# Optimization experiments

Measured on AMD Instinct MI355X. Metric: run time of the kernel, lower is better.

## Reference

```python
import jax, jax.numpy as jnp
import numpy as np

B, T, D, H, O = 256, 512, 256, 1024, 128


def setup_inputs() -> dict:
    key = jax.random.key(0)
    ks = jax.random.split(key, 16)
    s_x = 1.0 / np.sqrt(D)
    s_h = 1.0 / np.sqrt(H)
    def lin(k, shape, s):
        return jax.random.uniform(k, shape, jnp.float32, -s, s)
    return {
        "x": jax.random.normal(ks[0], (B, T, D), jnp.float32),
        "Wgx": lin(ks[1], (H, D), s_x), "bgx": lin(ks[2], (H,), s_x),
        "Wgh": lin(ks[3], (H, H), s_h),
        "Wix": lin(ks[4], (H, D), s_x), "bix": lin(ks[5], (H,), s_x),
        "Wih": lin(ks[6], (H, H), s_h),
        "Wfx": lin(ks[7], (H, D), s_x), "bfx": lin(ks[8], (H,), s_x),
        "Wfh": lin(ks[9], (H, H), s_h),
        "Wox": lin(ks[10], (H, D), s_x), "box": lin(ks[11], (H,), s_x),
        "Woh": lin(ks[12], (H, H), s_h),
        "Why": lin(ks[13], (O, H), s_h), "bhy": lin(ks[14], (O,), s_h),
    }


def _lstm_forward(x, Wgx, bgx, Wgh, Wix, bix, Wih, Wfx, bfx, Wfh, Wox, box, Woh, Why, bhy):
    # Precompute all input-side projections in one big GEMM: [B,T,4H]
    Wx = jnp.concatenate([Wgx, Wix, Wfx, Wox], axis=0)          # [4H, D]
    bx = jnp.concatenate([bgx, bix, bfx, box], axis=0)          # [4H]
    Wh = jnp.concatenate([Wgh, Wih, Wfh, Woh], axis=0)          # [4H, H]
    xz = jnp.einsum('btd,kd->tbk', x, Wx) + bx                  # [T,B,4H]

    Hd = Wgh.shape[0]

    def step(carry, xz_t):
        h, c = carry
        z = xz_t + h @ Wh.T                                     # [B,4H]
        g = jnp.tanh(z[:, :Hd])
        i = jax.nn.sigmoid(z[:, Hd:2 * Hd])
        f = jax.nn.sigmoid(z[:, 2 * Hd:3 * Hd])
        o = jax.nn.sigmoid(z[:, 3 * Hd:])
        c = g * i + c * f
        h = jnp.tanh(c) * o
        return (h, c), None

    h0 = jnp.zeros((x.shape[0], Hd), x.dtype)
    c0 = jnp.zeros((x.shape[0], Hd), x.dtype)
    (h, _), _ = jax.lax.scan(step, (h0, c0), xz)
    p = h @ Why.T + bhy
    return jax.nn.softmax(p, axis=-1)


def reference(x, Wgx, bgx, Wgh, Wix, bix, Wih, Wfx, bfx, Wfh, Wox, box, Woh, Why, bhy):
    return _lstm_forward(x, Wgx, bgx, Wgh, Wix, bix, Wih, Wfx, bfx, Wfh, Wox, box, Woh, Why, bhy)
```

## Files before the change

kernel.cpp:

```cpp
#include <hip/hip_runtime.h>
#include <math.h>

#define B_  256
#define T_  512
#define D_  256
#define H_  1024
#define O_  128
#define N4H 4096

typedef __attribute__((ext_vector_type(8))) short bf16x8;
typedef __attribute__((ext_vector_type(4))) float f32x4;

__device__ __forceinline__ unsigned short f2bf(float x) {
    union { float f; unsigned u; } v; v.f = x;
    unsigned r = v.u + 0x7fffu + ((v.u >> 16) & 1u);
    return (unsigned short)(r >> 16);
}
__device__ __forceinline__ float bf2f(unsigned short b) {
    union { float f; unsigned u; } v; v.u = ((unsigned)b) << 16;
    return v.f;
}
__device__ __forceinline__ void splitf(float w, short& hi, short& lo) {
    union { float f; unsigned u; } v; v.f = w;
    union { float f; unsigned u; } hf; hf.u = v.u & 0xffff0000u;
    hi = (short)(unsigned short)(v.u >> 16);
    lo = (short)f2bf(w - hf.f);
}

__device__ __forceinline__ void load_h_batch(
    const unsigned short* a0, const unsigned short* a1,
    const unsigned short* a2, const unsigned short* a3,
    const unsigned short* b0, const unsigned short* b1,
    const unsigned short* b2, const unsigned short* b3,
    bf16x8& r0, bf16x8& r1, bf16x8& r2, bf16x8& r3,
    bf16x8& r4, bf16x8& r5, bf16x8& r6, bf16x8& r7)
{
    asm volatile(
        "global_load_dwordx4 %0, %8, off sc0 sc1\n\t"
        "global_load_dwordx4 %1, %9, off sc0 sc1\n\t"
        "global_load_dwordx4 %2, %10, off sc0 sc1\n\t"
        "global_load_dwordx4 %3, %11, off sc0 sc1\n\t"
        "global_load_dwordx4 %4, %12, off sc0 sc1\n\t"
        "global_load_dwordx4 %5, %13, off sc0 sc1\n\t"
        "global_load_dwordx4 %6, %14, off sc0 sc1\n\t"
        "global_load_dwordx4 %7, %15, off sc0 sc1\n\t"
        "s_waitcnt vmcnt(0)"
        : "=&v"(r0), "=&v"(r1), "=&v"(r2), "=&v"(r3),
          "=&v"(r4), "=&v"(r5), "=&v"(r6), "=&v"(r7)
        : "v"(a0), "v"(a1), "v"(a2), "v"(a3),
          "v"(b0), "v"(b1), "v"(b2), "v"(b3)
        : "memory");
}

__device__ __forceinline__ void store_h4(unsigned short* p, unsigned int d) {
    asm volatile("global_store_dword %0, %1, off sc0 sc1"
                 :: "v"(p), "v"(d) : "memory");
}

__global__ __launch_bounds__(256) void pack_weights(
    const float* __restrict__ Wgx, const float* __restrict__ bgx, const float* __restrict__ Wgh,
    const float* __restrict__ Wix, const float* __restrict__ bix, const float* __restrict__ Wih,
    const float* __restrict__ Wfx, const float* __restrict__ bfx, const float* __restrict__ Wfh,
    const float* __restrict__ Wox, const float* __restrict__ box, const float* __restrict__ Woh,
    unsigned short* __restrict__ Whhi, unsigned short* __restrict__ Whlo,
    unsigned short* __restrict__ WXhi, unsigned short* __restrict__ WXlo,
    float* __restrict__ biasP)
{
    int idx = blockIdx.x * 256 + threadIdx.x;
    const int K = H_ + D_;
    const int total = N4H * K;
    if (idx < total) {
        int np = idx / K;
        int k  = idx - np * K;
        int j = np >> 2, g = np & 3;
        const float* Wh = (g == 0) ? Wgh : (g == 1) ? Wih : (g == 2) ? Wfh : Woh;
        const float* Wx = (g == 0) ? Wgx : (g == 1) ? Wix : (g == 2) ? Wfx : Wox;
        float w = (k < H_) ? Wh[j * H_ + k] : Wx[j * D_ + (k - H_)];
        unsigned short hi = f2bf(w);
        unsigned short lo = f2bf(w - bf2f(hi));
        if (k < H_) { Whhi[np * H_ + k] = hi; Whlo[np * H_ + k] = lo; }
        else        { WXhi[np * D_ + (k - H_)] = hi; WXlo[np * D_ + (k - H_)] = lo; }
    }
    if (idx < N4H) {
        int j = idx >> 2, g = idx & 3;
        const float* bx = (g == 0) ? bgx : (g == 1) ? bix : (g == 2) ? bfx : box;
        biasP[idx] = bx[j];
    }
}

__global__ __launch_bounds__(512, 2) void lstm_persistent(
    const float* __restrict__ x,
    const unsigned short* __restrict__ Whhi, const unsigned short* __restrict__ Whlo,
    const unsigned short* __restrict__ WXhi, const unsigned short* __restrict__ WXlo,
    const float* __restrict__ biasP,
    unsigned short* __restrict__ h0hi, unsigned short* __restrict__ h0lo,
    unsigned short* __restrict__ h1hi, unsigned short* __restrict__ h1lo,
    float* __restrict__ xz,
    unsigned int* __restrict__ bar,
    int Tc)
{
    __shared__ __align__(16) float zbuf[8][64][68];

    const int tid  = threadIdx.x;
    const int wave = tid >> 6;
    const int lane = tid & 63;
    const int lrow = lane & 15;
    const int quad = lane >> 4;

    const int fid = blockIdx.x;
    const int xcd = fid & 7;
    const int s   = fid >> 3;
    const int cgi = xcd * 8 + (s & 7);
    const int rg  = s >> 3;
    const int rbase = rg * 64;
    const int cbase = cgi * 64;

    const int b_loc = tid >> 3;
    const int oc    = (tid & 7) * 8;
    const int bown  = rbase + b_loc;
    const int j0    = cgi * 16 + (tid & 7) * 2;
    float c0 = 0.f, c1 = 0.f;

    unsigned int* const mybar = bar + rg * 32;
    unsigned int barTarget = 0;

    for (int t0 = 0; t0 < T_; t0 += Tc) {
        const int tc = (T_ - t0 < Tc) ? (T_ - t0) : Tc;

        for (int t_rel = wave; t_rel < tc; t_rel += 8) {
            const int t = t0 + t_rel;
            f32x4 acc[4][4];
            #pragma unroll
            for (int rs = 0; rs < 4; ++rs)
                #pragma unroll
                for (int cs = 0; cs < 4; ++cs)
                    acc[rs][cs] = (f32x4){0.f, 0.f, 0.f, 0.f};

            #pragma unroll 1
            for (int kc = 0; kc < D_; kc += 32) {
                bf16x8 Ahi[4], Alo[4], Bh[4], Bl[4];
                #pragma unroll
                for (int rs = 0; rs < 4; ++rs) {
                    int b = rbase + rs * 16 + lrow;
                    const float* p = x + (size_t)b * (T_ * D_) + (size_t)t * D_ + kc + quad * 8;
                    float4 v0 = *(const float4*)p;
                    float4 v1 = *(const float4*)(p + 4);
                    float vv[8] = {v0.x, v0.y, v0.z, v0.w, v1.x, v1.y, v1.z, v1.w};
                    #pragma unroll
                    for (int j = 0; j < 8; ++j) {
                        short hi, lo; splitf(vv[j], hi, lo);
                        Ahi[rs][j] = hi; Alo[rs][j] = lo;
                    }
                }
                #pragma unroll
                for (int cs = 0; cs < 4; ++cs) {
                    int off = (cbase + cs * 16 + lrow) * D_ + kc + quad * 8;
                    Bh[cs] = *(const bf16x8*)(WXhi + off);
                    Bl[cs] = *(const bf16x8*)(WXlo + off);
                }
                #pragma unroll
                for (int rs = 0; rs < 4; ++rs)
                    #pragma unroll
                    for (int cs = 0; cs < 4; ++cs) {
                        acc[rs][cs] = __builtin_amdgcn_mfma_f32_16x16x32_bf16(Ahi[rs], Bh[cs], acc[rs][cs], 0, 0, 0);
                        acc[rs][cs] = __builtin_amdgcn_mfma_f32_16x16x32_bf16(Ahi[rs], Bl[cs], acc[rs][cs], 0, 0, 0);
                        acc[rs][cs] = __builtin_amdgcn_mfma_f32_16x16x32_bf16(Alo[rs], Bh[cs], acc[rs][cs], 0, 0, 0);
                    }
            }
            #pragma unroll
            for (int cs = 0; cs < 4; ++cs) {
                int col = cbase + cs * 16 + lrow;
                float bv = biasP[col];
                #pragma unroll
                for (int rs = 0; rs < 4; ++rs) {
                    int row0 = rbase + rs * 16 + quad * 4;
                    #pragma unroll
                    for (int r = 0; r < 4; ++r)
                        xz[(size_t)(t_rel * B_ + row0 + r) * N4H + col] = acc[rs][cs][r] + bv;
                }
            }
        }

        for (int t_rel = 0; t_rel < tc; ++t_rel) {
            const int t = t0 + t_rel;
            const unsigned short* ih = (t & 1) ? h1hi : h0hi;
            const unsigned short* il = (t & 1) ? h1lo : h0lo;
            unsigned short* oh = (t & 1) ? h0hi : h1hi;
            unsigned short* ol = (t & 1) ? h0lo : h1lo;

            f32x4 acc[4][4];
            #pragma unroll
            for (int rs = 0; rs < 4; ++rs)
                #pragma unroll
                for (int cs = 0; cs < 4; ++cs)
                    acc[rs][cs] = (f32x4){0.f, 0.f, 0.f, 0.f};

            const int kb = wave * 128;
            #pragma unroll 1
            for (int kc = 0; kc < 128; kc += 32) {
                const int k = kb + kc + quad * 8;
                bf16x8 Ahi[4], Alo[4], Bh[4], Bl[4];
                #pragma unroll
                for (int cs = 0; cs < 4; ++cs) {
                    int off = (cbase + cs * 16 + lrow) * H_ + k;
                    Bh[cs] = *(const bf16x8*)(Whhi + off);
                    Bl[cs] = *(const bf16x8*)(Whlo + off);
                }
                const int r0o = (rbase + 0 * 16 + lrow) * H_ + k;
                const int r1o = (rbase + 1 * 16 + lrow) * H_ + k;
                const int r2o = (rbase + 2 * 16 + lrow) * H_ + k;
                const int r3o = (rbase + 3 * 16 + lrow) * H_ + k;
                load_h_batch(ih + r0o, ih + r1o, ih + r2o, ih + r3o,
                             il + r0o, il + r1o, il + r2o, il + r3o,
                             Ahi[0], Ahi[1], Ahi[2], Ahi[3],
                             Alo[0], Alo[1], Alo[2], Alo[3]);
                #pragma unroll
                for (int rs = 0; rs < 4; ++rs)
                    #pragma unroll
                    for (int cs = 0; cs < 4; ++cs) {
                        acc[rs][cs] = __builtin_amdgcn_mfma_f32_16x16x32_bf16(Ahi[rs], Bh[cs], acc[rs][cs], 0, 0, 0);
                        acc[rs][cs] = __builtin_amdgcn_mfma_f32_16x16x32_bf16(Ahi[rs], Bl[cs], acc[rs][cs], 0, 0, 0);
                        acc[rs][cs] = __builtin_amdgcn_mfma_f32_16x16x32_bf16(Alo[rs], Bh[cs], acc[rs][cs], 0, 0, 0);
                    }
            }

            #pragma unroll
            for (int rs = 0; rs < 4; ++rs)
                #pragma unroll
                for (int cs = 0; cs < 4; ++cs)
                    #pragma unroll
                    for (int r = 0; r < 4; ++r)
                        zbuf[wave][rs * 16 + quad * 4 + r][cs * 16 + lrow] = acc[rs][cs][r];
            __syncthreads();

            float zz[8];
            #pragma unroll
            for (int i = 0; i < 8; i += 4) {
                float s0 = 0.f, s1 = 0.f, s2 = 0.f, s3 = 0.f;
                #pragma unroll
                for (int w = 0; w < 8; ++w) {
                    float4 v = *(const float4*)&zbuf[w][b_loc][oc + i];
                    s0 += v.x; s1 += v.y; s2 += v.z; s3 += v.w;
                }
                zz[i] = s0; zz[i + 1] = s1; zz[i + 2] = s2; zz[i + 3] = s3;
            }

            const size_t xzoff = ((size_t)t_rel * B_ + bown) * N4H + cbase + oc;
            float4 xa = *(const float4*)(xz + xzoff);
            float4 xb = *(const float4*)(xz + xzoff + 4);
            zz[0] += xa.x; zz[1] += xa.y; zz[2] += xa.z; zz[3] += xa.w;
            zz[4] += xb.x; zz[5] += xb.y; zz[6] += xb.z; zz[7] += xb.w;

            float cold[2] = {c0, c1};
            unsigned short hh[2], hl[2];
            float cnew[2];
            #pragma unroll
            for (int j = 0; j < 2; ++j) {
                float zg = zz[4 * j + 0];
                float zi = zz[4 * j + 1];
                float zf = zz[4 * j + 2];
                float zo = zz[4 * j + 3];
                float g  = tanhf(zg);
                float ig = 1.f / (1.f + expf(-zi));
                float fg = 1.f / (1.f + expf(-zf));
                float og = 1.f / (1.f + expf(-zo));
                float cn = g * ig + cold[j] * fg;
                float hn = tanhf(cn) * og;
                cnew[j] = cn;
                unsigned short h16 = f2bf(hn);
                hh[j] = h16;
                hl[j] = f2bf(hn - bf2f(h16));
            }
            c0 = cnew[0]; c1 = cnew[1];
            store_h4(&oh[bown * H_ + j0], (unsigned)hh[0] | ((unsigned)hh[1] << 16));
            store_h4(&ol[bown * H_ + j0], (unsigned)hl[0] | ((unsigned)hl[1] << 16));

            __syncthreads();
            if (t != T_ - 1) {
                barTarget += 64;
                if (tid == 0) {
                    __hip_atomic_fetch_add(mybar, 1u, __ATOMIC_RELAXED,
                                           __HIP_MEMORY_SCOPE_AGENT);
                    while (__hip_atomic_load(mybar, __ATOMIC_RELAXED,
                                             __HIP_MEMORY_SCOPE_AGENT) < barTarget)
                        __builtin_amdgcn_s_sleep(1);
                }
                __syncthreads();
            }
        }
    }
}

__global__ __launch_bounds__(128) void final_proj(
    const unsigned short* __restrict__ hhi, const unsigned short* __restrict__ hlo,
    const float* __restrict__ Why, const float* __restrict__ bhy,
    float* __restrict__ out)
{
    __shared__ float hsh[H_];
    __shared__ float red[O_];
    const int b = blockIdx.x, tid = threadIdx.x;

    for (int k = tid; k < H_; k += O_)
        hsh[k] = bf2f(hhi[(size_t)b * H_ + k]) + bf2f(hlo[(size_t)b * H_ + k]);
    __syncthreads();

    float s = bhy[tid];
    const float* w = Why + (size_t)tid * H_;
    #pragma unroll 4
    for (int k = 0; k < H_; k += 4) {
        float4 wv = *(const float4*)(w + k);
        s += hsh[k] * wv.x + hsh[k + 1] * wv.y + hsh[k + 2] * wv.z + hsh[k + 3] * wv.w;
    }

    red[tid] = s; __syncthreads();
    for (int off = 64; off > 0; off >>= 1) {
        if (tid < off) red[tid] = fmaxf(red[tid], red[tid + off]);
        __syncthreads();
    }
    float mx = red[0]; __syncthreads();
    float e = expf(s - mx);
    red[tid] = e; __syncthreads();
    for (int off = 64; off > 0; off >>= 1) {
        if (tid < off) red[tid] += red[tid + off];
        __syncthreads();
    }
    out[(size_t)b * O_ + tid] = e / red[0];
}

extern "C" void kernel_launch(void* const* d_in, const int* in_sizes, int n_in,
                              void* d_out, int out_size, void* d_ws, size_t ws_size,
                              hipStream_t stream)
{
    const float* x   = (const float*)d_in[0];
    const float* Wgx = (const float*)d_in[1];
    const float* bgx = (const float*)d_in[2];
    const float* Wgh = (const float*)d_in[3];
    const float* Wix = (const float*)d_in[4];
    const float* bix = (const float*)d_in[5];
    const float* Wih = (const float*)d_in[6];
    const float* Wfx = (const float*)d_in[7];
    const float* bfx = (const float*)d_in[8];
    const float* Wfh = (const float*)d_in[9];
    const float* Wox = (const float*)d_in[10];
    const float* box = (const float*)d_in[11];
    const float* Woh = (const float*)d_in[12];
    const float* Why = (const float*)d_in[13];
    const float* bhy = (const float*)d_in[14];

    unsigned short* Whhi = (unsigned short*)d_ws;
    unsigned short* Whlo = Whhi + (size_t)N4H * H_;
    unsigned short* WXhi = Whlo + (size_t)N4H * H_;
    unsigned short* WXlo = WXhi + (size_t)N4H * D_;
    float*          bP   = (float*)(WXlo + (size_t)N4H * D_);
    unsigned int*   bars = (unsigned int*)(bP + N4H);
    unsigned short* hA_hi = (unsigned short*)(bars + 128);
    unsigned short* hA_lo = hA_hi + (size_t)B_ * H_;
    unsigned short* hB_hi = hA_lo + (size_t)B_ * H_;
    unsigned short* hB_lo = hB_hi + (size_t)B_ * H_;
    float*          xz    = (float*)(hB_lo + (size_t)B_ * H_);

    const size_t fixed_bytes = (size_t)((char*)xz - (char*)d_ws);
    const size_t per_t = (size_t)B_ * N4H * sizeof(float);
    int Tc = 1;
    if (ws_size > fixed_bytes) {
        size_t fit = (ws_size - fixed_bytes) / per_t;
        Tc = (fit > 32) ? 32 : (fit < 1 ? 1 : (int)fit);
    }

    hipMemsetAsync(bars, 0, 512 + (size_t)B_ * H_ * 4, stream);

    const int totalW = N4H * (H_ + D_);
    pack_weights<<<(totalW + 255) / 256, 256, 0, stream>>>(
        Wgx, bgx, Wgh, Wix, bix, Wih, Wfx, bfx, Wfh, Wox, box, Woh,
        Whhi, Whlo, WXhi, WXlo, bP);

    void* kargs[] = {
        (void*)&x, (void*)&Whhi, (void*)&Whlo, (void*)&WXhi, (void*)&WXlo,
        (void*)&bP, (void*)&hA_hi, (void*)&hA_lo, (void*)&hB_hi, (void*)&hB_lo,
        (void*)&xz, (void*)&bars, (void*)&Tc
    };
    hipLaunchCooperativeKernel((const void*)lstm_persistent,
                               dim3(256), dim3(512), kargs, 0, stream);

    final_proj<<<B_, 128, 0, stream>>>(hA_hi, hA_lo, Why, bhy, (float*)d_out);
}
```

Measured before the change: 11.67 ms.

## Overlap input projection with recurrent barrier wait and retile blocks to 32x128

The input-side projection for the next time chunk now runs in small units inside the per-step barrier wait, instead of as a separate phase before each chunk. The xz buffer is double-buffered to make this possible. Tiles change from 64 rows x 64 cols to 32 rows x 128 cols, so each barrier group has 32 blocks instead of 64. The aim is to hide projection work behind the grid-sync latency and shrink barrier fan-in, at the cost of twice the xz workspace, possibly a smaller Tc, and more register pressure.

```diff
diff --git a/kernel.cpp b/kernel.cpp
--- a/kernel.cpp
+++ b/kernel.cpp
@@ -27,34 +27,29 @@
     lo = (short)f2bf(w - hf.f);
 }
 
-__device__ __forceinline__ void load_h_batch(
+__device__ __forceinline__ void load_h4(
     const unsigned short* a0, const unsigned short* a1,
-    const unsigned short* a2, const unsigned short* a3,
     const unsigned short* b0, const unsigned short* b1,
-    const unsigned short* b2, const unsigned short* b3,
-    bf16x8& r0, bf16x8& r1, bf16x8& r2, bf16x8& r3,
-    bf16x8& r4, bf16x8& r5, bf16x8& r6, bf16x8& r7)
+    bf16x8& r0, bf16x8& r1, bf16x8& r2, bf16x8& r3)
 {
     asm volatile(
-        "global_load_dwordx4 %0, %8, off sc0 sc1\n\t"
-        "global_load_dwordx4 %1, %9, off sc0 sc1\n\t"
-        "global_load_dwordx4 %2, %10, off sc0 sc1\n\t"
-        "global_load_dwordx4 %3, %11, off sc0 sc1\n\t"
-        "global_load_dwordx4 %4, %12, off sc0 sc1\n\t"
-        "global_load_dwordx4 %5, %13, off sc0 sc1\n\t"
-        "global_load_dwordx4 %6, %14, off sc0 sc1\n\t"
-        "global_load_dwordx4 %7, %15, off sc0 sc1\n\t"
+        "global_load_dwordx4 %0, %4, off sc0 sc1\n\t"
+        "global_load_dwordx4 %1, %5, off sc0 sc1\n\t"
+        "global_load_dwordx4 %2, %6, off sc0 sc1\n\t"
+        "global_load_dwordx4 %3, %7, off sc0 sc1\n\t"
         "s_waitcnt vmcnt(0)"
-        : "=&v"(r0), "=&v"(r1), "=&v"(r2), "=&v"(r3),
-          "=&v"(r4), "=&v"(r5), "=&v"(r6), "=&v"(r7)
-        : "v"(a0), "v"(a1), "v"(a2), "v"(a3),
-          "v"(b0), "v"(b1), "v"(b2), "v"(b3)
+        : "=&v"(r0), "=&v"(r1), "=&v"(r2), "=&v"(r3)
+        : "v"(a0), "v"(a1), "v"(b0), "v"(b1)
         : "memory");
 }
 
 __device__ __forceinline__ void store_h4(unsigned short* p, unsigned int d) {
     asm volatile("global_store_dword %0, %1, off sc0 sc1"
                  :: "v"(p), "v"(d) : "memory");
+}
+
+__device__ __forceinline__ void drain_vmem() {
+    asm volatile("s_waitcnt vmcnt(0)" ::: "memory");
 }
 
 __global__ __launch_bounds__(256) void pack_weights(
@@ -88,6 +83,83 @@
     }
 }
 
+struct Prod {
+    int t;
+    int u;
+    f32x4 xa[2][4];
+};
+
+__device__ __forceinline__ void prod_zero(Prod& P) {
+    #pragma unroll
+    for (int rs = 0; rs < 2; ++rs)
+        #pragma unroll
+        for (int cs = 0; cs < 4; ++cs)
+            P.xa[rs][cs] = (f32x4){0.f, 0.f, 0.f, 0.f};
+}
+
+__device__ __forceinline__ void prod_unit(
+    Prod& P, int tcn, int nt0,
+    const float* __restrict__ x,
+    const unsigned short* __restrict__ WXhi,
+    const unsigned short* __restrict__ WXlo,
+    const float* __restrict__ biasP,
+    float* __restrict__ xzn,
+    int rbase, int cbase, int lrow, int quad)
+{
+    if (P.t >= tcn) return;
+    const int kc   = (P.u & 7) * 32;
+    const int half = P.u >> 3;
+    const int t    = nt0 + P.t;
+
+    bf16x8 Ahi[2], Alo[2];
+    #pragma unroll
+    for (int rs = 0; rs < 2; ++rs) {
+        int b = rbase + rs * 16 + lrow;
+        const float* p = x + (size_t)b * (T_ * D_) + (size_t)t * D_ + kc + quad * 8;
+        float4 v0 = *(const float4*)p;
+        float4 v1 = *(const float4*)(p + 4);
+        float vv[8] = {v0.x, v0.y, v0.z, v0.w, v1.x, v1.y, v1.z, v1.w};
+        #pragma unroll
+        for (int j = 0; j < 8; ++j) {
+            short hi, lo; splitf(vv[j], hi, lo);
+            Ahi[rs][j] = hi; Alo[rs][j] = lo;
+        }
+    }
+    bf16x8 Bh[4], Bl[4];
+    #pragma unroll
+    for (int cs = 0; cs < 4; ++cs) {
+        int off = (cbase + half * 64 + cs * 16 + lrow) * D_ + kc + quad * 8;
+        Bh[cs] = *(const bf16x8*)(WXhi + off);
+        Bl[cs] = *(const bf16x8*)(WXlo + off);
+    }
+    #pragma unroll
+    for (int rs = 0; rs < 2; ++rs)
+        #pragma unroll
+        for (int cs = 0; cs < 4; ++cs) {
+            P.xa[rs][cs] = __builtin_amdgcn_mfma_f32_16x16x32_bf16(Ahi[rs], Bh[cs], P.xa[rs][cs], 0, 0, 0);
+            P.xa[rs][cs] = __builtin_amdgcn_mfma_f32_16x16x32_bf16(Ahi[rs], Bl[cs], P.xa[rs][cs], 0, 0, 0);
+            P.xa[rs][cs] = __builtin_amdgcn_mfma_f32_16x16x32_bf16(Alo[rs], Bh[cs], P.xa[rs][cs], 0, 0, 0);
+        }
+
+    P.u += 1;
+    if ((P.u & 7) == 0) {
+        #pragma unroll
+        for (int cs = 0; cs < 4; ++cs) {
+            int col = cbase + half * 64 + cs * 16 + lrow;
+            float bv = biasP[col];
+            #pragma unroll
+            for (int rs = 0; rs < 2; ++rs) {
+                int row0 = rbase + rs * 16 + quad * 4;
+                #pragma unroll
+                for (int r = 0; r < 4; ++r)
+                    xzn[(size_t)(P.t * B_ + row0 + r) * N4H + col] = P.xa[rs][cs][r] + bv;
+            }
+        }
+        prod_zero(P);
+        if (P.u == 16) { P.u = 0; P.t += 8; }
+    }
+}
+
 __global__ __launch_bounds__(512, 2) void lstm_persistent(
     const float* __restrict__ x,
     const unsigned short* __restrict__ Whhi, const unsigned short* __restrict__ Whlo,
@@ -95,11 +167,11 @@
     const float* __restrict__ biasP,
     unsigned short* __restrict__ h0hi, unsigned short* __restrict__ h0lo,
     unsigned short* __restrict__ h1hi, unsigned short* __restrict__ h1lo,
-    float* __restrict__ xz,
+    float* xzA, float* xzB,
     unsigned int* __restrict__ bar,
     int Tc)
 {
-    __shared__ __align__(16) float zbuf[8][64][68];
+    __shared__ __align__(16) float zbuf[8][32][132];
 
     const int tid  = threadIdx.x;
     const int wave = tid >> 6;
@@ -110,124 +182,94 @@
     const int fid = blockIdx.x;
     const int xcd = fid & 7;
     const int s   = fid >> 3;
-    const int cgi = xcd * 8 + (s & 7);
-    const int rg  = s >> 3;
-    const int rbase = rg * 64;
-    const int cbase = cgi * 64;
-
-    const int b_loc = tid >> 3;
-    const int oc    = (tid & 7) * 8;
+    const int cgi = xcd * 4 + (s & 3);
+    const int rg  = s >> 2;
+    const int rbase = rg * 32;
+    const int cbase = cgi * 128;
+
+    const int b_loc = tid >> 4;
+    const int cq    = tid & 15;
+    const int oc    = cq * 8;
     const int bown  = rbase + b_loc;
-    const int j0    = cgi * 16 + (tid & 7) * 2;
+    const int j0    = cgi * 32 + cq * 2;
     float c0 = 0.f, c1 = 0.f;
 
     unsigned int* const mybar = bar + rg * 32;
     unsigned int barTarget = 0;
 
-    for (int t0 = 0; t0 < T_; t0 += Tc) {
-        const int tc = (T_ - t0 < Tc) ? (T_ - t0) : Tc;
-
-        for (int t_rel = wave; t_rel < tc; t_rel += 8) {
-            const int t = t0 + t_rel;
-            f32x4 acc[4][4];
+    int t0 = 0, cur = 0;
+    int tcc = (Tc < T_) ? Tc : T_;
+
+    {
+        Prod P; P.t = wave; P.u = 0; prod_zero(P);
+        while (P.t < tcc)
+            prod_unit(P, tcc, 0, x, WXhi, WXlo, biasP, xzA,
+                      rbase, cbase, lrow, quad);
+    }
+    __syncthreads();
+
+    while (true) {
+        const int nt0 = t0 + tcc;
+        const int tcn = (nt0 < T_) ? ((T_ - nt0 < Tc) ? T_ - nt0 : Tc) : 0;
+        float* const xzc = cur ? xzB : xzA;
+        float* const xzn = cur ? xzA : xzB;
+
+        Prod P; P.t = wave; P.u = 0; prod_zero(P);
+        const int ntiles = (tcn > wave) ? ((tcn - wave + 7) >> 3) : 0;
+        const int units  = ntiles * 16;
+        const int Q      = (units + tcc - 1) / tcc;
+
+        for (int tr = 0; tr < tcc; ++tr) {
+            const int t = t0 + tr;
+            const unsigned short* ih = (t & 1) ? h1hi : h0hi;
+            const unsigned short* il = (t & 1) ? h1lo : h0lo;
+            unsigned short* oh = (t & 1) ? h0hi : h1hi;
+            unsigned short* ol = (t & 1) ? h0lo : h1lo;
+
+            f32x4 acc[2][8];
             #pragma unroll
-            for (int rs = 0; rs < 4; ++rs)
-                #pragma unroll
-                for (int cs = 0; cs < 4; ++cs)
+            for (int rs = 0; rs < 2; ++rs)
+                #pragma unroll
+                for (int cs = 0; cs < 8; ++cs)
                     acc[rs][cs] = (f32x4){0.f, 0.f, 0.f, 0.f};
 
+            const int kb = wave * 128;
             #pragma unroll 1
-            for (int kc = 0; kc < D_; kc += 32) {
-                bf16x8 Ahi[4], Alo[4], Bh[4], Bl[4];
-                #pragma unroll
-                for (int rs = 0; rs < 4; ++rs) {
-                    int b = rbase + rs * 16 + lrow;
-                    const float* p = x + (size_t)b * (T_ * D_) + (size_t)t * D_ + kc + quad * 8;
-                    float4 v0 = *(const float4*)p;
-                    float4 v1 = *(const float4*)(p + 4);
-                    float vv[8] = {v0.x, v0.y, v0.z, v0.w, v1.x, v1.y, v1.z, v1.w};
+            for (int kc4 = 0; kc4 < 4; ++kc4) {
+                const int k = kb + kc4 * 32 + quad * 8;
+                bf16x8 Ahi[2], Alo[2], Bh[8], Bl[8];
+                #pragma unroll
+                for (int cs = 0; cs < 4; ++cs) {
+                    int off = (cbase + cs * 16 + lrow) * H_ + k;
+                    Bh[cs] = *(const bf16x8*)(Whhi + off);
+                    Bl[cs] = *(const bf16x8*)(Whlo + off);
+                }
+                {
+                    int o0 = (rbase + 0 * 16 + lrow) * H_ + k;
+                    int o1 = (rbase + 1 * 16 + lrow) * H_ + k;
+                    load_h4(ih + o0, ih + o1, il + o0, il + o1,
+                            Ahi[0], Ahi[1], Alo[0], Alo[1]);
+                }
+                #pragma unroll
+                for (int cs = 4; cs < 8; ++cs) {
+                    int off = (cbase + cs * 16 + lrow) * H_ + k;
+                    Bh[cs] = *(const bf16x8*)(Whhi + off);
+                    Bl[cs] = *(const bf16x8*)(Whlo + off);
+                }
+                #pragma unroll
+                for (int rs = 0; rs < 2; ++rs)
                     #pragma unroll
-                    for (int j = 0; j < 8; ++j) {
-                        short hi, lo; splitf(vv[j], hi, lo);
-                        Ahi[rs][j] = hi; Alo[rs][j] = lo;
-                    }
-                }
-                #pragma unroll
-                for (int cs = 0; cs < 4; ++cs) {
-                    int off = (cbase + cs * 16 + lrow) * D_ + kc + quad * 8;
-                    Bh[cs] = *(const bf16x8*)(WXhi + off);
-                    Bl[cs] = *(const bf16x8*)(WXlo + off);
-                }
-                #pragma unroll
-                for (int rs = 0; rs < 4; ++rs)
-                    #pragma unroll
-                    for (int cs = 0; cs < 4; ++cs) {
+                    for (int cs = 0; cs < 8; ++cs) {
                         acc[rs][cs] = __builtin_amdgcn_mfma_f32_16x16x32_bf16(Ahi[rs], Bh[cs], acc[rs][cs], 0, 0, 0);
                         acc[rs][cs] = __builtin_amdgcn_mfma_f32_16x16x32_bf16(Ahi[rs], Bl[cs], acc[rs][cs], 0, 0, 0);
                         acc[rs][cs] = __builtin_amdgcn_mfma_f32_16x16x32_bf16(Alo[rs], Bh[cs], acc[rs][cs], 0, 0, 0);
                     }
             }
+
             #pragma unroll
-            for (int cs = 0; cs < 4; ++cs) {
-                int col = cbase + cs * 16 + lrow;
-                float bv = biasP[col];
-                #pragma unroll
-                for (int rs = 0; rs < 4; ++rs) {
-                    int row0 = rbase + rs * 16 + quad * 4;
-                    #pragma unroll
-                    for (int r = 0; r < 4; ++r)
-                        xz[(size_t)(t_rel * B_ + row0 + r) * N4H + col] = acc[rs][cs][r] + bv;
-                }
-            }
-        }
-
-        for (int t_rel = 0; t_rel < tc; ++t_rel) {
-            const int t = t0 + t_rel;
-            const unsigned short* ih = (t & 1) ? h1hi : h0hi;
-            const unsigned short* il = (t & 1) ? h1lo : h0lo;
-            unsigned short* oh = (t & 1) ? h0hi : h1hi;
-            unsigned short* ol = (t & 1) ? h0lo : h1lo;
-
-            f32x4 acc[4][4];
-            #pragma unroll
-            for (int rs = 0; rs < 4; ++rs)
-                #pragma unroll
-                for (int cs = 0; cs < 4; ++cs)
-                    acc[rs][cs] = (f32x4){0.f, 0.f, 0.f, 0.f};
-
-            const int kb = wave * 128;
-            #pragma unroll 1
-            for (int kc = 0; kc < 128; kc += 32) {
-                const int k = kb + kc + quad * 8;
-                bf16x8 Ahi[4], Alo[4], Bh[4], Bl[4];
-                #pragma unroll
-                for (int cs = 0; cs < 4; ++cs) {
-                    int off = (cbase + cs * 16 + lrow) * H_ + k;
-                    Bh[cs] = *(const bf16x8*)(Whhi + off);
-                    Bl[cs] = *(const bf16x8*)(Whlo + off);
-                }
-                const int r0o = (rbase + 0 * 16 + lrow) * H_ + k;
-                const int r1o = (rbase + 1 * 16 + lrow) * H_ + k;
-                const int r2o = (rbase + 2 * 16 + lrow) * H_ + k;
-                const int r3o = (rbase + 3 * 16 + lrow) * H_ + k;
-                load_h_batch(ih + r0o, ih + r1o, ih + r2o, ih + r3o,
-                             il + r0o, il + r1o, il + r2o, il + r3o,
-                             Ahi[0], Ahi[1], Ahi[2], Ahi[3],
-                             Alo[0], Alo[1], Alo[2], Alo[3]);
-                #pragma unroll
-                for (int rs = 0; rs < 4; ++rs)
-                    #pragma unroll
-                    for (int cs = 0; cs < 4; ++cs) {
-                        acc[rs][cs] = __builtin_amdgcn_mfma_f32_16x16x32_bf16(Ahi[rs], Bh[cs], acc[rs][cs], 0, 0, 0);
-                        acc[rs][cs] = __builtin_amdgcn_mfma_f32_16x16x32_bf16(Ahi[rs], Bl[cs], acc[rs][cs], 0, 0, 0);
-                        acc[rs][cs] = __builtin_amdgcn_mfma_f32_16x16x32_bf16(Alo[rs], Bh[cs], acc[rs][cs], 0, 0, 0);
-                    }
-            }
-
-            #pragma unroll
-            for (int rs = 0; rs < 4; ++rs)
-                #pragma unroll
-                for (int cs = 0; cs < 4; ++cs)
+            for (int rs = 0; rs < 2; ++rs)
+                #pragma unroll
+                for (int cs = 0; cs < 8; ++cs)
                     #pragma unroll
                     for (int r = 0; r < 4; ++r)
                         zbuf[wave][rs * 16 + quad * 4 + r][cs * 16 + lrow] = acc[rs][cs][r];
@@ -245,9 +287,9 @@
                 zz[i] = s0; zz[i + 1] = s1; zz[i + 2] = s2; zz[i + 3] = s3;
             }
 
-            const size_t xzoff = ((size_t)t_rel * B_ + bown) * N4H + cbase + oc;
-            float4 xa = *(const float4*)(xz + xzoff);
-            float4 xb = *(const float4*)(xz + xzoff + 4);
+            const size_t xzoff = ((size_t)tr * B_ + bown) * N4H + cbase + oc;
+            float4 xa = *(const float4*)(xzc + xzoff);
+            float4 xb = *(const float4*)(xzc + xzoff + 4);
             zz[0] += xa.x; zz[1] += xa.y; zz[2] += xa.z; zz[3] += xa.w;
             zz[4] += xb.x; zz[5] += xb.y; zz[6] += xb.z; zz[7] += xb.w;
 
@@ -275,12 +317,18 @@
             store_h4(&oh[bown * H_ + j0], (unsigned)hh[0] | ((unsigned)hh[1] << 16));
             store_h4(&ol[bown * H_ + j0], (unsigned)hl[0] | ((unsigned)hl[1] << 16));
 
+            drain_vmem();
             __syncthreads();
+
             if (t != T_ - 1) {
-                barTarget += 64;
-                if (tid == 0) {
+                barTarget += 32;
+                if (tid == 0)
                     __hip_atomic_fetch_add(mybar, 1u, __ATOMIC_RELAXED,
                                            __HIP_MEMORY_SCOPE_AGENT);
+                for (int q = 0; q < Q; ++q)
+                    prod_unit(P, tcn, nt0, x, WXhi, WXlo, biasP, xzn,
+                              rbase, cbase, lrow, quad);
+                if (tid == 0) {
                     while (__hip_atomic_load(mybar, __ATOMIC_RELAXED,
                                              __HIP_MEMORY_SCOPE_AGENT) < barTarget)
                         __builtin_amdgcn_s_sleep(1);
@@ -288,6 +336,9 @@
                 __syncthreads();
             }
         }
+
+        if (tcn == 0) break;
+        t0 = nt0; tcc = tcn; cur ^= 1;
     }
 }
 
@@ -353,21 +404,23 @@
     unsigned short* WXlo = WXhi + (size_t)N4H * D_;
     float*          bP   = (float*)(WXlo + (size_t)N4H * D_);
     unsigned int*   bars = (unsigned int*)(bP + N4H);
-    unsigned short* hA_hi = (unsigned short*)(bars + 128);
+    unsigned short* hA_hi = (unsigned short*)(bars + 1024);
     unsigned short* hA_lo = hA_hi + (size_t)B_ * H_;
     unsigned short* hB_hi = hA_lo + (size_t)B_ * H_;
     unsigned short* hB_lo = hB_hi + (size_t)B_ * H_;
-    float*          xz    = (float*)(hB_lo + (size_t)B_ * H_);
-
-    const size_t fixed_bytes = (size_t)((char*)xz - (char*)d_ws);
+    float*          xzBase = (float*)(hB_lo + (size_t)B_ * H_);
+
+    const size_t fixed_bytes = (size_t)((char*)xzBase - (char*)d_ws);
     const size_t per_t = (size_t)B_ * N4H * sizeof(float);
     int Tc = 1;
     if (ws_size > fixed_bytes) {
-        size_t fit = (ws_size - fixed_bytes) / per_t;
+        size_t fit = (ws_size - fixed_bytes) / (2 * per_t);
         Tc = (fit > 32) ? 32 : (fit < 1 ? 1 : (int)fit);
     }
-
-    hipMemsetAsync(bars, 0, 512 + (size_t)B_ * H_ * 4, stream);
+    float* xzA = xzBase;
+    float* xzB = xzBase + (size_t)Tc * B_ * N4H;
+
+    hipMemsetAsync(bars, 0, 4096 + (size_t)B_ * H_ * 4, stream);
 
     const int totalW = N4H * (H_ + D_);
     pack_weights<<<(totalW + 255) / 256, 256, 0, stream>>>(
@@ -377,7 +430,7 @@
     void* kargs[] = {
         (void*)&x, (void*)&Whhi, (void*)&Whlo, (void*)&WXhi, (void*)&WXlo,
         (void*)&bP, (void*)&hA_hi, (void*)&hA_lo, (void*)&hB_hi, (void*)&hB_lo,
-        (void*)&xz, (void*)&bars, (void*)&Tc
+        (void*)&xzA, (void*)&xzB, (void*)&bars, (void*)&Tc
     };
     hipLaunchCooperativeKernel((const void*)lstm_persistent,
                                dim3(256), dim3(512), kargs, 0, stream);
```

Result: slower. 13.61 ms (+16.6%).

## Retile LSTM recurrence to 32x128 blocks with LDS-staged h and per-block flags

Applied to the files above, without the earlier changes.

Each workgroup now owns 32 batch rows by 128 gate columns instead of 64x64. Each wave computes the full K=1024 reduction for its own 16 columns, so the cross-wave LDS reduction is gone. The h tile is staged once into swizzled LDS per step, and the atomic-counter barrier becomes per-block flag stores that wave 0 polls in parallel. The aim is to cut h global reloads, cross-wave reduction traffic and atomic contention on the per-step critical path. The cost is a larger LDS footprint and a flag scheme that relies on store visibility ordering.

```diff
diff --git a/kernel.cpp b/kernel.cpp
--- a/kernel.cpp
+++ b/kernel.cpp
@@ -27,28 +27,43 @@
     lo = (short)f2bf(w - hf.f);
 }
 
-__device__ __forceinline__ void load_h_batch(
-    const unsigned short* a0, const unsigned short* a1,
-    const unsigned short* a2, const unsigned short* a3,
-    const unsigned short* b0, const unsigned short* b1,
-    const unsigned short* b2, const unsigned short* b3,
+__device__ __forceinline__ void ld8_nowait(
+    const unsigned short* p,
     bf16x8& r0, bf16x8& r1, bf16x8& r2, bf16x8& r3,
     bf16x8& r4, bf16x8& r5, bf16x8& r6, bf16x8& r7)
 {
     asm volatile(
         "global_load_dwordx4 %0, %8, off sc0 sc1\n\t"
-        "global_load_dwordx4 %1, %9, off sc0 sc1\n\t"
-        "global_load_dwordx4 %2, %10, off sc0 sc1\n\t"
-        "global_load_dwordx4 %3, %11, off sc0 sc1\n\t"
-        "global_load_dwordx4 %4, %12, off sc0 sc1\n\t"
-        "global_load_dwordx4 %5, %13, off sc0 sc1\n\t"
-        "global_load_dwordx4 %6, %14, off sc0 sc1\n\t"
-        "global_load_dwordx4 %7, %15, off sc0 sc1\n\t"
+        "global_load_dwordx4 %1, %8, off offset:256 sc0 sc1\n\t"
+        "global_load_dwordx4 %2, %8, off offset:512 sc0 sc1\n\t"
+        "global_load_dwordx4 %3, %8, off offset:768 sc0 sc1\n\t"
+        "global_load_dwordx4 %4, %8, off offset:1024 sc0 sc1\n\t"
+        "global_load_dwordx4 %5, %8, off offset:1280 sc0 sc1\n\t"
+        "global_load_dwordx4 %6, %8, off offset:1536 sc0 sc1\n\t"
+        "global_load_dwordx4 %7, %8, off offset:1792 sc0 sc1"
+        : "=&v"(r0), "=&v"(r1), "=&v"(r2), "=&v"(r3),
+          "=&v"(r4), "=&v"(r5), "=&v"(r6), "=&v"(r7)
+        : "v"(p)
+        : "memory");
+}
+__device__ __forceinline__ void ld8_wait(
+    const unsigned short* p,
+    bf16x8& r0, bf16x8& r1, bf16x8& r2, bf16x8& r3,
+    bf16x8& r4, bf16x8& r5, bf16x8& r6, bf16x8& r7)
+{
+    asm volatile(
+        "global_load_dwordx4 %0, %8, off sc0 sc1\n\t"
+        "global_load_dwordx4 %1, %8, off offset:256 sc0 sc1\n\t"
+        "global_load_dwordx4 %2, %8, off offset:512 sc0 sc1\n\t"
+        "global_load_dwordx4 %3, %8, off offset:768 sc0 sc1\n\t"
+        "global_load_dwordx4 %4, %8, off offset:1024 sc0 sc1\n\t"
+        "global_load_dwordx4 %5, %8, off offset:1280 sc0 sc1\n\t"
+        "global_load_dwordx4 %6, %8, off offset:1536 sc0 sc1\n\t"
+        "global_load_dwordx4 %7, %8, off offset:1792 sc0 sc1\n\t"
         "s_waitcnt vmcnt(0)"
         : "=&v"(r0), "=&v"(r1), "=&v"(r2), "=&v"(r3),
           "=&v"(r4), "=&v"(r5), "=&v"(r6), "=&v"(r7)
-        : "v"(a0), "v"(a1), "v"(a2), "v"(a3),
-          "v"(b0), "v"(b1), "v"(b2), "v"(b3)
+        : "v"(p)
         : "memory");
 }
 
@@ -56,6 +71,21 @@
     asm volatile("global_store_dword %0, %1, off sc0 sc1"
                  :: "v"(p), "v"(d) : "memory");
 }
+__device__ __forceinline__ unsigned ld_flag(const unsigned* p) {
+    unsigned v;
+    asm volatile("global_load_dword %0, %1, off sc0 sc1\n\ts_waitcnt vmcnt(0)"
+                 : "=v"(v) : "v"(p) : "memory");
+    return v;
+}
+__device__ __forceinline__ void st_flag(unsigned* p, unsigned v) {
+    asm volatile("global_store_dword %0, %1, off sc0 sc1"
+                 :: "v"(p), "v"(v) : "memory");
+}
+__device__ __forceinline__ void drain_vmem() {
+    asm volatile("s_waitcnt vmcnt(0)" ::: "memory");
+}
+
+#define HIDX(k8, row) (((((k8) * 32) + (row)) * 8) ^ (((k8) & 7) * 8))
 
 __global__ __launch_bounds__(256) void pack_weights(
     const float* __restrict__ Wgx, const float* __restrict__ bgx, const float* __restrict__ Wgh,
@@ -96,10 +126,12 @@
     unsigned short* __restrict__ h0hi, unsigned short* __restrict__ h0lo,
     unsigned short* __restrict__ h1hi, unsigned short* __restrict__ h1lo,
     float* __restrict__ xz,
-    unsigned int* __restrict__ bar,
+    unsigned int* __restrict__ flg,
     int Tc)
 {
-    __shared__ __align__(16) float zbuf[8][64][68];
+    __shared__ __align__(16) unsigned short hsHI[32768];
+    __shared__ __align__(16) unsigned short hsLO[32768];
+    __shared__ __align__(16) float zsc[8][32][20];
 
     const int tid  = threadIdx.x;
     const int wave = tid >> 6;
@@ -110,150 +142,164 @@
     const int fid = blockIdx.x;
     const int xcd = fid & 7;
     const int s   = fid >> 3;
-    const int cgi = xcd * 8 + (s & 7);
-    const int rg  = s >> 3;
-    const int rbase = rg * 64;
-    const int cbase = cgi * 64;
-
-    const int b_loc = tid >> 3;
-    const int oc    = (tid & 7) * 8;
-    const int bown  = rbase + b_loc;
-    const int j0    = cgi * 16 + (tid & 7) * 2;
+    const int cgi = xcd * 4 + (s & 3);
+    const int rg  = s >> 2;
+    const int rbase = rg * 32;
+    const int cbase = cgi * 128;
+
+    const int srow = (tid >> 2) & 31;
+    const int sks  = (tid & 3) | (((tid >> 7) & 3) << 2);
+
+    const int erow = lane >> 1;
+    const int eps  = lane & 1;
+    const int bown = rbase + erow;
+    const int j0   = cgi * 32 + wave * 4 + eps * 2;
     float c0 = 0.f, c1 = 0.f;
 
-    unsigned int* const mybar = bar + rg * 32;
-    unsigned int barTarget = 0;
+    unsigned int* const myflag = flg + rg * 32 + cgi;
+    const unsigned int* const pollbase = flg + rg * 32;
 
     for (int t0 = 0; t0 < T_; t0 += Tc) {
         const int tc = (T_ - t0 < Tc) ? (T_ - t0) : Tc;
 
-        for (int t_rel = wave; t_rel < tc; t_rel += 8) {
-            const int t = t0 + t_rel;
-            f32x4 acc[4][4];
-            #pragma unroll
-            for (int rs = 0; rs < 4; ++rs)
+        for (int tr = wave; tr < tc; tr += 8) {
+            const int t = t0 + tr;
+            #pragma unroll 1
+            for (int hf = 0; hf < 2; ++hf) {
+                f32x4 xacc[2][4];
                 #pragma unroll
-                for (int cs = 0; cs < 4; ++cs)
-                    acc[rs][cs] = (f32x4){0.f, 0.f, 0.f, 0.f};
-
-            #pragma unroll 1
-            for (int kc = 0; kc < D_; kc += 32) {
-                bf16x8 Ahi[4], Alo[4], Bh[4], Bl[4];
-                #pragma unroll
-                for (int rs = 0; rs < 4; ++rs) {
-                    int b = rbase + rs * 16 + lrow;
-                    const float* p = x + (size_t)b * (T_ * D_) + (size_t)t * D_ + kc + quad * 8;
-                    float4 v0 = *(const float4*)p;
-                    float4 v1 = *(const float4*)(p + 4);
-                    float vv[8] = {v0.x, v0.y, v0.z, v0.w, v1.x, v1.y, v1.z, v1.w};
+                for (int rs = 0; rs < 2; ++rs)
                     #pragma unroll
-                    for (int j = 0; j < 8; ++j) {
-                        short hi, lo; splitf(vv[j], hi, lo);
-                        Ahi[rs][j] = hi; Alo[rs][j] = lo;
+                    for (int cs = 0; cs < 4; ++cs)
+                        xacc[rs][cs] = (f32x4){0.f, 0.f, 0.f, 0.f};
+                #pragma unroll 1
+                for (int kc = 0; kc < 8; ++kc) {
+                    const int kx = kc * 32 + quad * 8;
+                    bf16x8 Ahi[2], Alo[2];
+                    #pragma unroll
+                    for (int rs = 0; rs < 2; ++rs) {
+                        const float* p = x + (size_t)(rbase + rs * 16 + lrow) * (T_ * D_)
+                                           + (size_t)t * D_ + kx;
+                        float4 v0 = *(const float4*)p;
+                        float4 v1 = *(const float4*)(p + 4);
+                        float vv[8] = {v0.x, v0.y, v0.z, v0.w, v1.x, v1.y, v1.z, v1.w};
+                        #pragma unroll
+                        for (int j = 0; j < 8; ++j) {
+                            short hi, lo; splitf(vv[j], hi, lo);
+                            Ahi[rs][j] = hi; Alo[rs][j] = lo;
+                        }
                     }
+                    bf16x8 Bh[4], Bl[4];
+                    #pragma unroll
+                    for (int cs = 0; cs < 4; ++cs) {
+                        size_t off = (size_t)(cbase + hf * 64 + cs * 16 + lrow) * D_ + kx;
+                        Bh[cs] = *(const bf16x8*)(WXhi + off);
+                        Bl[cs] = *(const bf16x8*)(WXlo + off);
+                    }
+                    #pragma unroll
+                    for (int rs = 0; rs < 2; ++rs)
+                        #pragma unroll
+                        for (int cs = 0; cs < 4; ++cs) {
+                            xacc[rs][cs] = __builtin_amdgcn_mfma_f32_16x16x32_bf16(Ahi[rs], Bh[cs], xacc[rs][cs], 0, 0, 0);
+                            xacc[rs][cs] = __builtin_amdgcn_mfma_f32_16x16x32_bf16(Ahi[rs], Bl[cs], xacc[rs][cs], 0, 0, 0);
+                            xacc[rs][cs] = __builtin_amdgcn_mfma_f32_16x16x32_bf16(Alo[rs], Bh[cs], xacc[rs][cs], 0, 0, 0);
+                        }
                 }
                 #pragma unroll
                 for (int cs = 0; cs < 4; ++cs) {
-                    int off = (cbase + cs * 16 + lrow) * D_ + kc + quad * 8;
-                    Bh[cs] = *(const bf16x8*)(WXhi + off);
-                    Bl[cs] = *(const bf16x8*)(WXlo + off);
+                    int col = cbase + hf * 64 + cs * 16 + lrow;
+                    float bv = biasP[col];
+                    #pragma unroll
+                    for (int rs = 0; rs < 2; ++rs) {
+                        int row0 = rbase + rs * 16 + quad * 4;
+                        #pragma unroll
+                        for (int r = 0; r < 4; ++r)
+                            xz[(size_t)(tr * B_ + row0 + r) * N4H + col] = xacc[rs][cs][r] + bv;
+                    }
                 }
-                #pragma unroll
-                for (int rs = 0; rs < 4; ++rs)
-                    #pragma unroll
-                    for (int cs = 0; cs < 4; ++cs) {
-                        acc[rs][cs] = __builtin_amdgcn_mfma_f32_16x16x32_bf16(Ahi[rs], Bh[cs], acc[rs][cs], 0, 0, 0);
-                        acc[rs][cs] = __builtin_amdgcn_mfma_f32_16x16x32_bf16(Ahi[rs], Bl[cs], acc[rs][cs], 0, 0, 0);
-                        acc[rs][cs] = __builtin_amdgcn_mfma_f32_16x16x32_bf16(Alo[rs], Bh[cs], acc[rs][cs], 0, 0, 0);
-                    }
-            }
-            #pragma unroll
-            for (int cs = 0; cs < 4; ++cs) {
-                int col = cbase + cs * 16 + lrow;
-                float bv = biasP[col];
-                #pragma unroll
-                for (int rs = 0; rs < 4; ++rs) {
-                    int row0 = rbase + rs * 16 + quad * 4;
-                    #pragma unroll
-                    for (int r = 0; r < 4; ++r)
-                        xz[(size_t)(t_rel * B_ + row0 + r) * N4H + col] = acc[rs][cs][r] + bv;
-                }
             }
         }
-
-        for (int t_rel = 0; t_rel < tc; ++t_rel) {
-            const int t = t0 + t_rel;
+        __syncthreads();
+
+        for (int tr = 0; tr < tc; ++tr) {
+            const int t = t0 + tr;
             const unsigned short* ih = (t & 1) ? h1hi : h0hi;
             const unsigned short* il = (t & 1) ? h1lo : h0lo;
             unsigned short* oh = (t & 1) ? h0hi : h1hi;
             unsigned short* ol = (t & 1) ? h0lo : h1lo;
 
-            f32x4 acc[4][4];
+            {
+                const unsigned short* phi = ih + (size_t)(rbase + srow) * H_ + sks * 8;
+                const unsigned short* plo = il + (size_t)(rbase + srow) * H_ + sks * 8;
+                bf16x8 H0, H1, H2, H3, H4, H5, H6, H7;
+                bf16x8 L0, L1, L2, L3, L4, L5, L6, L7;
+                ld8_nowait(phi, H0, H1, H2, H3, H4, H5, H6, H7);
+                ld8_wait  (plo, L0, L1, L2, L3, L4, L5, L6, L7);
+                *(bf16x8*)&hsHI[HIDX(sks +   0, srow)] = H0;
+                *(bf16x8*)&hsHI[HIDX(sks +  16, srow)] = H1;
+                *(bf16x8*)&hsHI[HIDX(sks +  32, srow)] = H2;
+                *(bf16x8*)&hsHI[HIDX(sks +  48, srow)] = H3;
+                *(bf16x8*)&hsHI[HIDX(sks +  64, srow)] = H4;
+                *(bf16x8*)&hsHI[HIDX(sks +  80, srow)] = H5;
+                *(bf16x8*)&hsHI[HIDX(sks +  96, srow)] = H6;
+                *(bf16x8*)&hsHI[HIDX(sks + 112, srow)] = H7;
+                *(bf16x8*)&hsLO[HIDX(sks +   0, srow)] = L0;
+                *(bf16x8*)&hsLO[HIDX(sks +  16, srow)] = L1;
+                *(bf16x8*)&hsLO[HIDX(sks +  32, srow)] = L2;
+                *(bf16x8*)&hsLO[HIDX(sks +  48, srow)] = L3;
+                *(bf16x8*)&hsLO[HIDX(sks +  64, srow)] = L4;
+                *(bf16x8*)&hsLO[HIDX(sks +  80, srow)] = L5;
+                *(bf16x8*)&hsLO[HIDX(sks +  96, srow)] = L6;
+                *(bf16x8*)&hsLO[HIDX(sks + 112, srow)] = L7;
+            }
+            __syncthreads();
+
+            f32x4 aH0 = (f32x4){0.f,0.f,0.f,0.f}, aL0 = aH0, aX0 = aH0;
+            f32x4 aH1 = aH0, aL1 = aH0, aX1 = aH0;
+            {
+                const unsigned short* wbh = Whhi + (size_t)(cbase + wave * 16 + lrow) * H_ + quad * 8;
+                const unsigned short* wbl = Whlo + (size_t)(cbase + wave * 16 + lrow) * H_ + quad * 8;
+                #pragma unroll 4
+                for (int kc = 0; kc < 32; ++kc) {
+                    const int k8 = kc * 4 + quad;
+                    bf16x8 Bh = *(const bf16x8*)(wbh + kc * 32);
+                    bf16x8 Bl = *(const bf16x8*)(wbl + kc * 32);
+                    bf16x8 Ah0 = *(const bf16x8*)&hsHI[HIDX(k8, lrow)];
+                    bf16x8 Ah1 = *(const bf16x8*)&hsHI[HIDX(k8, 16 + lrow)];
+                    bf16x8 Al0 = *(const bf16x8*)&hsLO[HIDX(k8, lrow)];
+                    bf16x8 Al1 = *(const bf16x8*)&hsLO[HIDX(k8, 16 + lrow)];
+                    aH0 = __builtin_amdgcn_mfma_f32_16x16x32_bf16(Ah0, Bh, aH0, 0, 0, 0);
+                    aL0 = __builtin_amdgcn_mfma_f32_16x16x32_bf16(Ah0, Bl, aL0, 0, 0, 0);
+                    aX0 = __builtin_amdgcn_mfma_f32_16x16x32_bf16(Al0, Bh, aX0, 0, 0, 0);
+                    aH1 = __builtin_amdgcn_mfma_f32_16x16x32_bf16(Ah1, Bh, aH1, 0, 0, 0);
+                    aL1 = __builtin_amdgcn_mfma_f32_16x16x32_bf16(Ah1, Bl, aL1, 0, 0, 0);
+                    aX1 = __builtin_amdgcn_mfma_f32_16x16x32_bf16(Al1, Bh, aX1, 0, 0, 0);
+                }
+            }
+            f32x4 a0 = aH0 + aL0 + aX0;
+            f32x4 a1 = aH1 + aL1 + aX1;
+
             #pragma unroll
-            for (int rs = 0; rs < 4; ++rs)
-                #pragma unroll
-                for (int cs = 0; cs < 4; ++cs)
-                    acc[rs][cs] = (f32x4){0.f, 0.f, 0.f, 0.f};
-
-            const int kb = wave * 128;
-            #pragma unroll 1
-            for (int kc = 0; kc < 128; kc += 32) {
-                const int k = kb + kc + quad * 8;
-                bf16x8 Ahi[4], Alo[4], Bh[4], Bl[4];
-                #pragma unroll
-                for (int cs = 0; cs < 4; ++cs) {
-                    int off = (cbase + cs * 16 + lrow) * H_ + k;
-                    Bh[cs] = *(const bf16x8*)(Whhi + off);
-                    Bl[cs] = *(const bf16x8*)(Whlo + off);
-                }
-                const int r0o = (rbase + 0 * 16 + lrow) * H_ + k;
-                const int r1o = (rbase + 1 * 16 + lrow) * H_ + k;
-                const int r2o = (rbase + 2 * 16 + lrow) * H_ + k;
-                const int r3o = (rbase + 3 * 16 + lrow) * H_ + k;
-                load_h_batch(ih + r0o, ih + r1o, ih + r2o, ih + r3o,
-                             il + r0o, il + r1o, il + r2o, il + r3o,
-                             Ahi[0], Ahi[1], Ahi[2], Ahi[3],
-                             Alo[0], Alo[1], Alo[2], Alo[3]);
-                #pragma unroll
-                for (int rs = 0; rs < 4; ++rs)
-                    #pragma unroll
-                    for (int cs = 0; cs < 4; ++cs) {
-                        acc[rs][cs] = __builtin_amdgcn_mfma_f32_16x16x32_bf16(Ahi[rs], Bh[cs], acc[rs][cs], 0, 0, 0);
-                        acc[rs][cs] = __builtin_amdgcn_mfma_f32_16x16x32_bf16(Ahi[rs], Bl[cs], acc[rs][cs], 0, 0, 0);
-                        acc[rs][cs] = __builtin_amdgcn_mfma_f32_16x16x32_bf16(Alo[rs], Bh[cs], acc[rs][cs], 0, 0, 0);
-                    }
-            }
-
-            #pragma unroll
-            for (int rs = 0; rs < 4; ++rs)
-                #pragma unroll
-                for (int cs = 0; cs < 4; ++cs)
-                    #pragma unroll
-                    for (int r = 0; r < 4; ++r)
-                        zbuf[wave][rs * 16 + quad * 4 + r][cs * 16 + lrow] = acc[rs][cs][r];
-            __syncthreads();
-
+            for (int r = 0; r < 4; ++r) {
+                zsc[wave][quad * 4 + r][lrow] = a0[r];
+                zsc[wave][16 + quad * 4 + r][lrow] = a1[r];
+            }
             float zz[8];
-            #pragma unroll
-            for (int i = 0; i < 8; i += 4) {
-                float s0 = 0.f, s1 = 0.f, s2 = 0.f, s3 = 0.f;
-                #pragma unroll
-                for (int w = 0; w < 8; ++w) {
-                    float4 v = *(const float4*)&zbuf[w][b_loc][oc + i];
-                    s0 += v.x; s1 += v.y; s2 += v.z; s3 += v.w;
-                }
-                zz[i] = s0; zz[i + 1] = s1; zz[i + 2] = s2; zz[i + 3] = s3;
-            }
-
-            const size_t xzoff = ((size_t)t_rel * B_ + bown) * N4H + cbase + oc;
+            {
+                float4 v0 = *(const float4*)&zsc[wave][erow][eps * 8];
+                float4 v1 = *(const float4*)&zsc[wave][erow][eps * 8 + 4];
+                zz[0] = v0.x; zz[1] = v0.y; zz[2] = v0.z; zz[3] = v0.w;
+                zz[4] = v1.x; zz[5] = v1.y; zz[6] = v1.z; zz[7] = v1.w;
+            }
+            const size_t xzoff = ((size_t)tr * B_ + bown) * N4H + cbase + wave * 16 + eps * 8;
             float4 xa = *(const float4*)(xz + xzoff);
             float4 xb = *(const float4*)(xz + xzoff + 4);
             zz[0] += xa.x; zz[1] += xa.y; zz[2] += xa.z; zz[3] += xa.w;
             zz[4] += xb.x; zz[5] += xb.y; zz[6] += xb.z; zz[7] += xb.w;
 
             float cold[2] = {c0, c1};
+            float cnew[2];
             unsigned short hh[2], hl[2];
-            float cnew[2];
             #pragma unroll
             for (int j = 0; j < 2; ++j) {
                 float zg = zz[4 * j + 0];
@@ -272,18 +318,18 @@
                 hl[j] = f2bf(hn - bf2f(h16));
             }
             c0 = cnew[0]; c1 = cnew[1];
-            store_h4(&oh[bown * H_ + j0], (unsigned)hh[0] | ((unsigned)hh[1] << 16));
-            store_h4(&ol[bown * H_ + j0], (unsigned)hl[0] | ((unsigned)hl[1] << 16));
-
+            store_h4(&oh[(size_t)bown * H_ + j0], (unsigned)hh[0] | ((unsigned)hh[1] << 16));
+            store_h4(&ol[(size_t)bown * H_ + j0], (unsigned)hl[0] | ((unsigned)hl[1] << 16));
+
+            drain_vmem();
             __syncthreads();
+
             if (t != T_ - 1) {
-                barTarget += 64;
-                if (tid == 0) {
-                    __hip_atomic_fetch_add(mybar, 1u, __ATOMIC_RELAXED,
-                                           __HIP_MEMORY_SCOPE_AGENT);
-                    while (__hip_atomic_load(mybar, __ATOMIC_RELAXED,
-                                             __HIP_MEMORY_SCOPE_AGENT) < barTarget)
-                        __builtin_amdgcn_s_sleep(1);
+                const unsigned want = (unsigned)(t + 1);
+                if (tid == 0) st_flag(myflag, want);
+                if (wave == 0) {
+                    const unsigned* fp = pollbase + (lane & 31);
+                    while (ld_flag(fp) < want) __builtin_amdgcn_s_sleep(2);
                 }
                 __syncthreads();
             }
@@ -352,8 +398,8 @@
     unsigned short* WXhi = Whlo + (size_t)N4H * H_;
     unsigned short* WXlo = WXhi + (size_t)N4H * D_;
     float*          bP   = (float*)(WXlo + (size_t)N4H * D_);
-    unsigned int*   bars = (unsigned int*)(bP + N4H);
-    unsigned short* hA_hi = (unsigned short*)(bars + 128);
+    unsigned int*   flgs = (unsigned int*)(bP + N4H);
+    unsigned short* hA_hi = (unsigned short*)(flgs + 1024);
     unsigned short* hA_lo = hA_hi + (size_t)B_ * H_;
     unsigned short* hB_hi = hA_lo + (size_t)B_ * H_;
     unsigned short* hB_lo = hB_hi + (size_t)B_ * H_;
@@ -367,7 +413,7 @@
         Tc = (fit > 32) ? 32 : (fit < 1 ? 1 : (int)fit);
     }
 
-    hipMemsetAsync(bars, 0, 512 + (size_t)B_ * H_ * 4, stream);
+    hipMemsetAsync(flgs, 0, 4096 + (size_t)B_ * H_ * 4, stream);
 
     const int totalW = N4H * (H_ + D_);
     pack_weights<<<(totalW + 255) / 256, 256, 0, stream>>>(
@@ -377,7 +423,7 @@
     void* kargs[] = {
         (void*)&x, (void*)&Whhi, (void*)&Whlo, (void*)&WXhi, (void*)&WXlo,
         (void*)&bP, (void*)&hA_hi, (void*)&hA_lo, (void*)&hB_hi, (void*)&hB_lo,
-        (void*)&xz, (void*)&bars, (void*)&Tc
+        (void*)&xz, (void*)&flgs, (void*)&Tc
     };
     hipLaunchCooperativeKernel((const void*)lstm_persistent,
                                dim3(256), dim3(512), kargs, 0, stream);
```

Result: slower. 13.34 ms (+14.3%).
